# Performance work log

Measured on AMD Instinct MI355X. Metric: run time of the kernel, lower is better.

The kernel has to match this reference:

```python
import jax, jax.numpy as jnp
import numpy as np

H, C = 8, 16           # heads, per-head channels
NEG_SLOPE = 0.2        # PyG GATConv leaky_relu slope
N_NODES, N_EDGES, F_IN, N_GRAPHS = 50000, 600000, 64, 500


def setup_inputs() -> dict:
    key = jax.random.key(0)
    ks = jax.random.split(key, 24)
    s = 0.1  # weight init scale
    inp = {
        "x": jax.random.normal(ks[0], (N_NODES, F_IN), jnp.float32),
        "edge_index": jax.random.randint(ks[1], (2, N_EDGES), 0, N_NODES, dtype=jnp.int64),
        "batch": jnp.sort(jax.random.randint(ks[2], (N_NODES,), 0, N_GRAPHS, dtype=jnp.int64)),
        "W1": jax.random.normal(ks[3], (F_IN, H * C), jnp.float32) * s,
        "as1": jax.random.normal(ks[4], (H, C), jnp.float32) * s,
        "ad1": jax.random.normal(ks[5], (H, C), jnp.float32) * s,
        "b1": jnp.zeros((H * C,), jnp.float32),
        "W2": jax.random.normal(ks[6], (H * C, H * C), jnp.float32) * s,
        "as2": jax.random.normal(ks[7], (H, C), jnp.float32) * s,
        "ad2": jax.random.normal(ks[8], (H, C), jnp.float32) * s,
        "b2": jnp.zeros((H * C,), jnp.float32),
        "W3": jax.random.normal(ks[9], (H * C, H * C), jnp.float32) * s,
        "as3": jax.random.normal(ks[10], (H, C), jnp.float32) * s,
        "ad3": jax.random.normal(ks[11], (H, C), jnp.float32) * s,
        "b3": jnp.zeros((H * C,), jnp.float32),
        "fc1_w": jax.random.normal(ks[12], (H * C, 10), jnp.float32) * s,
        "fc1_b": jnp.zeros((10,), jnp.float32),
        "fc2_w": jax.random.normal(ks[13], (10, 1), jnp.float32) * s,
        "fc2_b": jnp.zeros((1,), jnp.float32),
    }
    return inp


def gat_layer(x, src, dst, W, att_src, att_dst, bias, n):
    # x: [N, F_in] -> h: [N, H, C]
    h = (x @ W).reshape(n, H, C)
    a_src = jnp.sum(h * att_src, axis=-1)  # [N, H]
    a_dst = jnp.sum(h * att_dst, axis=-1)  # [N, H]
    e = jax.nn.leaky_relu(a_src[src] + a_dst[dst], NEG_SLOPE)  # [E, H]
    # per-destination segment softmax (numerically stable)
    m = jax.ops.segment_max(e, dst, num_segments=n)            # [N, H]
    e = jnp.exp(e - m[dst])
    z = jax.ops.segment_sum(e, dst, num_segments=n)            # [N, H]
    alpha = e / (z[dst] + 1e-16)                               # [E, H]
    out = jax.ops.segment_sum(h[src] * alpha[:, :, None], dst, num_segments=n)  # [N, H, C]
    return out.reshape(n, H * C) + bias


def reference(x, edge_index, batch, W1, as1, ad1, b1, W2, as2, ad2, b2,
              W3, as3, ad3, b3, fc1_w, fc1_b, fc2_w, fc2_b):
    n = x.shape[0]
    # PyG GATConv default add_self_loops=True
    loop = jnp.arange(n, dtype=edge_index.dtype)
    src = jnp.concatenate([edge_index[0], loop])
    dst = jnp.concatenate([edge_index[1], loop])

    x = jax.nn.relu(gat_layer(x, src, dst, W1, as1, ad1, b1, n))
    x = jax.nn.relu(gat_layer(x, src, dst, W2, as2, ad2, b2, n))
    x = jax.nn.relu(gat_layer(x, src, dst, W3, as3, ad3, b3, n))

    # global_mean_pool over graphs
    sums = jax.ops.segment_sum(x, batch, num_segments=N_GRAPHS)          # [G, 128]
    cnts = jax.ops.segment_sum(jnp.ones((n,), x.dtype), batch, num_segments=N_GRAPHS)
    pooled = sums / jnp.maximum(cnts, 1.0)[:, None]

    hdn = jax.nn.relu(pooled @ fc1_w + fc1_b)
    return hdn @ fc2_w + fc2_b  # [G, 1]
```

## Files before the change

### kernel.cpp

```cpp
#include <hip/hip_runtime.h>
#include <hip/hip_bf16.h>

#define H 8
#define C 16
#define HC 128
#define NEG_SLOPE 0.2f

__global__ void init_kernel(int* __restrict__ deg8, int n) {
    int i = blockIdx.x * 256 + threadIdx.x;
    if (i < n) deg8[i] = 0;
}

__global__ void hist8_gptr_kernel(const int* __restrict__ ei, const int* __restrict__ batch,
                                  int* __restrict__ deg8, int* __restrict__ gptr,
                                  int E, int N, int G) {
    int t = blockIdx.x * 256 + threadIdx.x;
    int* dg = deg8 + (size_t)(blockIdx.x & 7) * N;
    int e0 = t * 4;
    if (e0 + 3 < E) {
        int4 d4 = *(const int4*)(ei + E + e0);
        atomicAdd(&dg[d4.x], 1);
        atomicAdd(&dg[d4.y], 1);
        atomicAdd(&dg[d4.z], 1);
        atomicAdd(&dg[d4.w], 1);
    } else if (e0 < E) {
        for (int j = e0; j < E; ++j) atomicAdd(&dg[ei[E + j]], 1);
    }
    int n0 = t * 4;
    if (n0 < N) {
        int v0 = batch[n0];
        int v1 = (n0 + 1 < N) ? batch[n0 + 1] : v0;
        int v2 = (n0 + 2 < N) ? batch[n0 + 2] : v1;
        int v3 = (n0 + 3 < N) ? batch[n0 + 3] : v2;
        int vals[4] = {v0, v1, v2, v3};
        int prev = (n0 == 0) ? -1 : batch[n0 - 1];
        for (int j = 0; j < 4; ++j) {
            int i = n0 + j;
            if (i >= N) break;
            int cur = vals[j];
            if (cur != prev)
                for (int g = prev + 1; g <= cur; ++g) gptr[g] = i;
            if (i == N - 1)
                for (int g = cur + 1; g <= G; ++g) gptr[g] = N;
            prev = cur;
        }
    }
}

__global__ void deg_reduce_kernel(const int* __restrict__ deg8, int* __restrict__ deg, int N) {
    int d = blockIdx.x * 256 + threadIdx.x;
    if (d >= N) return;
    int s = 1;
#pragma unroll
    for (int c = 0; c < 8; ++c) s += deg8[(size_t)c * N + d];
    deg[d] = s;
}

__global__ void scan_blk_kernel(const int* __restrict__ a, int* __restrict__ o,
                                int* __restrict__ p, int n) {
    __shared__ int sh[256];
    int tid = threadIdx.x;
    int base = blockIdx.x * 1024 + tid * 4;
    int4 v = make_int4(0, 0, 0, 0);
    if (base + 3 < n) v = *(const int4*)(a + base);
    else {
        if (base < n)     v.x = a[base];
        if (base + 1 < n) v.y = a[base + 1];
        if (base + 2 < n) v.z = a[base + 2];
        if (base + 3 < n) v.w = a[base + 3];
    }
    v.x = (v.x + 7) & ~7; v.y = (v.y + 7) & ~7; v.z = (v.z + 7) & ~7; v.w = (v.w + 7) & ~7;
    if (base >= n)     v.x = 0;
    if (base + 1 >= n) v.y = 0;
    if (base + 2 >= n) v.z = 0;
    if (base + 3 >= n) v.w = 0;
    int s = v.x + v.y + v.z + v.w;
    sh[tid] = s;
    __syncthreads();
    for (int off = 1; off < 256; off <<= 1) {
        int t = (tid >= off) ? sh[tid - off] : 0;
        __syncthreads();
        sh[tid] += t;
        __syncthreads();
    }
    int excl = sh[tid] - s;
    int4 ov;
    ov.x = excl; ov.y = ov.x + v.x; ov.z = ov.y + v.y; ov.w = ov.z + v.z;
    if (base + 3 < n) *(int4*)(o + base) = ov;
    else {
        if (base < n)     o[base] = ov.x;
        if (base + 1 < n) o[base + 1] = ov.y;
        if (base + 2 < n) o[base + 2] = ov.z;
        if (base + 3 < n) o[base + 3] = ov.w;
    }
    if (tid == 255) p[blockIdx.x] = sh[255];
}

__global__ void scan_part_kernel(int* __restrict__ p, int* __restrict__ tot, int nb) {
    __shared__ int sh[256];
    int tid = threadIdx.x;
    int v = (tid < nb) ? p[tid] : 0;
    sh[tid] = v;
    __syncthreads();
    for (int off = 1; off < 256; off <<= 1) {
        int t = (tid >= off) ? sh[tid - off] : 0;
        __syncthreads();
        sh[tid] += t;
        __syncthreads();
    }
    if (tid < nb) p[tid] = sh[tid] - v;
    if (tid == 255) *tot = sh[255];
}

__global__ void scan_add_kernel(int* __restrict__ o, const int* __restrict__ p, int n) {
    int off = p[blockIdx.x];
    int base = blockIdx.x * 1024 + threadIdx.x * 4;
    if (base + 3 < n) {
        int4 v = *(const int4*)(o + base);
        v.x += off; v.y += off; v.z += off; v.w += off;
        *(int4*)(o + base) = v;
    } else {
        if (base < n)     o[base] += off;
        if (base + 1 < n) o[base + 1] += off;
        if (base + 2 < n) o[base + 2] += off;
        if (base + 3 < n) o[base + 3] += off;
    }
}

__global__ void base_fill_kernel(int* __restrict__ deg8 ,
                                 const int* __restrict__ rowptr, int* __restrict__ csr, int N) {
    int d = blockIdx.x * 256 + threadIdx.x;
    if (d >= N) return;
    int base = rowptr[d];
    csr[base] = d;
    int run = base + 1;
    int cnt[8];
#pragma unroll
    for (int c = 0; c < 8; ++c) cnt[c] = deg8[(size_t)c * N + d];
#pragma unroll
    for (int c = 0; c < 8; ++c) { deg8[(size_t)c * N + d] = run; run += cnt[c]; }
    int rend = rowptr[d + 1];
    for (int p = run; p < rend; ++p) csr[p] = N;
    if (d == 0) {
        int tot = rowptr[N];
        for (int k = 0; k < 64; ++k) csr[tot + k] = N;
    }
}

__global__ void scatter8_kernel(const int* __restrict__ ei, int* __restrict__ base8,
                                int* __restrict__ csr, int E, int N) {
    int t = blockIdx.x * 256 + threadIdx.x;
    int* cur = base8 + (size_t)(blockIdx.x & 7) * N;
    int e0 = t * 4;
    if (e0 + 3 < E) {
        int4 s4 = *(const int4*)(ei + e0);
        int4 d4 = *(const int4*)(ei + E + e0);
        int p;
        p = atomicAdd(&cur[d4.x], 1); csr[p] = s4.x;
        p = atomicAdd(&cur[d4.y], 1); csr[p] = s4.y;
        p = atomicAdd(&cur[d4.z], 1); csr[p] = s4.z;
        p = atomicAdd(&cur[d4.w], 1); csr[p] = s4.w;
    } else if (e0 < E) {
        for (int j = e0; j < E; ++j) {
            int p = atomicAdd(&cur[ei[E + j]], 1);
            csr[p] = ei[j];
        }
    }
}

template <int K>
__global__ void gemm_att_kernel(const float* __restrict__ x, const float* __restrict__ W,
                                const float* __restrict__ as_, const float* __restrict__ ad_,
                                float* __restrict__ h, float* __restrict__ asrc,
                                float* __restrict__ adst, int n) {
    const int ROWS = 64;
    __shared__ float xs[ROWS][HC];
    int tx = threadIdx.x & 31;
    int ty = threadIdx.x >> 5;
    int row0 = blockIdx.x * ROWS;

    if (blockIdx.x == 0) {
        if (threadIdx.x < HC) h[(size_t)n * HC + threadIdx.x] = 0.f;
        if (threadIdx.x < H)  asrc[(size_t)n * H + threadIdx.x] = -INFINITY;
    }

    const int NV = ROWS * K / 4;
    for (int idx = threadIdx.x; idx < NV; idx += 256) {
        int rr = idx / (K / 4), kk = idx % (K / 4);
        int gr = row0 + rr;
        float4 v = (gr < n) ? ((const float4*)(x + (size_t)gr * K))[kk]
                            : make_float4(0.f, 0.f, 0.f, 0.f);
        *(float4*)(&xs[rr][kk * 4]) = v;
    }
    __syncthreads();

    const float* Wc = W + tx * 4;
    float acc[8][4];
#pragma unroll
    for (int r = 0; r < 8; ++r)
#pragma unroll
        for (int c = 0; c < 4; ++c) acc[r][c] = 0.f;

    for (int k = 0; k < K; k += 4) {
        float4 wv[4];
#pragma unroll
        for (int kk = 0; kk < 4; ++kk)
            wv[kk] = *(const float4*)(Wc + (size_t)(k + kk) * HC);
#pragma unroll
        for (int r = 0; r < 8; ++r) {
            float4 xr = *(const float4*)(&xs[ty * 8 + r][k]);
            acc[r][0] = fmaf(xr.x, wv[0].x, acc[r][0]);
            acc[r][1] = fmaf(xr.x, wv[0].y, acc[r][1]);
            acc[r][2] = fmaf(xr.x, wv[0].z, acc[r][2]);
            acc[r][3] = fmaf(xr.x, wv[0].w, acc[r][3]);
            acc[r][0] = fmaf(xr.y, wv[1].x, acc[r][0]);
            acc[r][1] = fmaf(xr.y, wv[1].y, acc[r][1]);
            acc[r][2] = fmaf(xr.y, wv[1].z, acc[r][2]);
            acc[r][3] = fmaf(xr.y, wv[1].w, acc[r][3]);
            acc[r][0] = fmaf(xr.z, wv[2].x, acc[r][0]);
            acc[r][1] = fmaf(xr.z, wv[2].y, acc[r][1]);
            acc[r][2] = fmaf(xr.z, wv[2].z, acc[r][2]);
            acc[r][3] = fmaf(xr.z, wv[2].w, acc[r][3]);
            acc[r][0] = fmaf(xr.w, wv[3].x, acc[r][0]);
            acc[r][1] = fmaf(xr.w, wv[3].y, acc[r][1]);
            acc[r][2] = fmaf(xr.w, wv[3].z, acc[r][2]);
            acc[r][3] = fmaf(xr.w, wv[3].w, acc[r][3]);
        }
    }
    __syncthreads();
#pragma unroll
    for (int r = 0; r < 8; ++r) {
        float4 o = make_float4(acc[r][0], acc[r][1], acc[r][2], acc[r][3]);
        *(float4*)(&xs[ty * 8 + r][tx * 4]) = o;
        int row = row0 + ty * 8 + r;
        if (row < n) *(float4*)(h + (size_t)row * HC + tx * 4) = o;
    }
    __syncthreads();

#pragma unroll
    for (int rep = 0; rep < 2; ++rep) {
        int pidx = threadIdx.x + rep * 256;
        int row = pidx >> 3;
        int hd = pidx & 7;
        if (row0 + row < n) {
            const float4* hv = (const float4*)&xs[row][hd * 16];
            const float4* sv = (const float4*)(as_ + hd * 16);
            const float4* dv = (const float4*)(ad_ + hd * 16);
            float s = 0.f, d = 0.f;
#pragma unroll
            for (int j = 0; j < 4; ++j) {
                float4 a = hv[j], u = sv[j], v = dv[j];
                s += a.x * u.x + a.y * u.y + a.z * u.z + a.w * u.w;
                d += a.x * v.x + a.y * v.y + a.z * v.z + a.w * v.w;
            }
            asrc[(size_t)(row0 + row) * H + hd] = s;
            adst[(size_t)(row0 + row) * H + hd] = d;
        }
    }
}

__global__ void gat_agg_kernel(const int* __restrict__ rowptr, const int* __restrict__ csr_src,
                               const float* __restrict__ h, const float* __restrict__ asrc,
                               const float* __restrict__ adst, const float* __restrict__ bias,
                               float* __restrict__ out, int N) {
    int dst = (blockIdx.x * 256 + threadIdx.x) >> 6;
    if (dst >= N) return;
    int lane = threadIdx.x & 63;
    int hd = lane >> 3;
    int beg = rowptr[dst], end = rowptr[dst + 1];
    float ad = adst[(size_t)dst * H + hd];
    const float2* h2 = (const float2*)h;

    float z = 0.f, a0 = 0.f, a1 = 0.f;
    int i0, i1, i2, i3, i4, i5, i6, i7;
    float e0, e1, e2, e3, e4, e5, e6, e7;
    float2 v0, v1, v2, v3, v4, v5, v6, v7;

#define LOADI(S, J) i##S = csr_src[(J)];
#define LOADV(S)                                                           \
    { e##S = asrc[(size_t)i##S * H + hd]; v##S = h2[(size_t)i##S * 64 + lane]; }
#define PROCE(S)                                                           \
    {   float e = e##S + ad;                                               \
        e = e > 0.f ? e : NEG_SLOPE * e;                                   \
        float w = __expf(e);                                               \
        z += w;                                                            \
        a0 = fmaf(w, v##S.x, a0);                                          \
        a1 = fmaf(w, v##S.y, a1);                                          \
    }
    LOADI(0, beg)     LOADI(1, beg + 1) LOADI(2, beg + 2) LOADI(3, beg + 3)
    LOADI(4, beg + 4) LOADI(5, beg + 5) LOADI(6, beg + 6) LOADI(7, beg + 7)
    LOADV(0) LOADV(1) LOADV(2) LOADV(3) LOADV(4) LOADV(5) LOADV(6) LOADV(7)
    LOADI(0, beg + 8)  LOADI(1, beg + 9)  LOADI(2, beg + 10) LOADI(3, beg + 11)
    LOADI(4, beg + 12) LOADI(5, beg + 13) LOADI(6, beg + 14) LOADI(7, beg + 15)

    for (int j = beg; j < end; j += 8) {
        PROCE(0) LOADV(0)
        PROCE(1) LOADV(1)
        PROCE(2) LOADV(2)
        PROCE(3) LOADV(3)
        PROCE(4) LOADV(4)
        PROCE(5) LOADV(5)
        PROCE(6) LOADV(6)
        PROCE(7) LOADV(7)
        LOADI(0, j + 16) LOADI(1, j + 17) LOADI(2, j + 18) LOADI(3, j + 19)
        LOADI(4, j + 20) LOADI(5, j + 21) LOADI(6, j + 22) LOADI(7, j + 23)
    }
#undef LOADI
#undef LOADV
#undef PROCE
    float inv = 1.f / (z + 1e-16f);
    int c2 = lane * 2;
    float r0 = fmaxf(a0 * inv + bias[c2], 0.f);
    float r1 = fmaxf(a1 * inv + bias[c2 + 1], 0.f);
    *(float2*)(out + (size_t)dst * HC + c2) = make_float2(r0, r1);
}

__global__ void pool_mlp_kernel(const float* __restrict__ x, const int* __restrict__ gptr,
                                const float* __restrict__ fc1w, const float* __restrict__ fc1b,
                                const float* __restrict__ fc2w, const float* __restrict__ fc2b,
                                float* __restrict__ out, int G) {
    __shared__ float sp[HC];
    __shared__ float sh[10];
    int g = blockIdx.x;
    int c = threadIdx.x;
    int beg = gptr[g], end = gptr[g + 1];
    float acc = 0.f;
    for (int n = beg; n < end; ++n) acc += x[(size_t)n * HC + c];
    sp[c] = acc / fmaxf((float)(end - beg), 1.f);
    __syncthreads();
    if (c < 10) {
        float s = fc1b[c];
        for (int k = 0; k < HC; ++k) s = fmaf(sp[k], fc1w[k * 10 + c], s);
        sh[c] = fmaxf(s, 0.f);
    }
    __syncthreads();
    if (c == 0) {
        float o = fc2b[0];
#pragma unroll
        for (int j = 0; j < 10; ++j) o = fmaf(sh[j], fc2w[j], o);
        out[g] = o;
    }
}

extern "C" void kernel_launch(void* const* d_in, const int* in_sizes, int n_in,
                              void* d_out, int out_size, void* d_ws, size_t ws_size,
                              hipStream_t stream) {
    const int N = in_sizes[0] / 64;
    const int E = in_sizes[1] / 2;
    const int G = out_size;
    const int CSR_CAP = E + 8 * N + 64;

    const float* x     = (const float*)d_in[0];
    const int*   ei    = (const int*)d_in[1];
    const int*   batch = (const int*)d_in[2];
    const float* W1 = (const float*)d_in[3];
    const float* as1 = (const float*)d_in[4];
    const float* ad1 = (const float*)d_in[5];
    const float* b1 = (const float*)d_in[6];
    const float* W2 = (const float*)d_in[7];
    const float* as2 = (const float*)d_in[8];
    const float* ad2 = (const float*)d_in[9];
    const float* b2 = (const float*)d_in[10];
    const float* W3 = (const float*)d_in[11];
    const float* as3 = (const float*)d_in[12];
    const float* ad3 = (const float*)d_in[13];
    const float* b3 = (const float*)d_in[14];
    const float* fc1w = (const float*)d_in[15];
    const float* fc1b = (const float*)d_in[16];
    const float* fc2w = (const float*)d_in[17];
    const float* fc2b = (const float*)d_in[18];

    float* ws = (float*)d_ws;
    float* h    = ws;
    float* xb0  = h + (size_t)(N + 1) * HC;
    float* xb1  = xb0 + (size_t)N * HC;
    float* asrc = xb1 + (size_t)N * HC;
    float* adst = asrc + (size_t)(N + 1) * H;
    int* ints   = (int*)(adst + (size_t)N * H);
    int* deg8   = ints;
    int* deg    = deg8 + (size_t)8 * N;
    int* rowptr = deg + N;
    int* gptr   = rowptr + N + 16;
    int* partN  = gptr + G + 16;
    int* csr    = partN + 256;

    dim3 blk(256);
    int grid4   = ((E + 3) / 4 + 255) / 256;
    int grid_n  = (N + 255) / 256;
    int grid_agg = (N * 64 + 255) / 256;
    int nbN = (N + 1023) / 1024;

    init_kernel<<<(8 * N + 255) / 256, blk, 0, stream>>>(deg8, 8 * N);
    hist8_gptr_kernel<<<grid4, blk, 0, stream>>>(ei, batch, deg8, gptr, E, N, G);
    deg_reduce_kernel<<<grid_n, blk, 0, stream>>>(deg8, deg, N);
    scan_blk_kernel<<<nbN, blk, 0, stream>>>(deg, rowptr, partN, N);
    scan_part_kernel<<<1, blk, 0, stream>>>(partN, rowptr + N, nbN);
    scan_add_kernel<<<nbN, blk, 0, stream>>>(rowptr, partN, N);
    base_fill_kernel<<<grid_n, blk, 0, stream>>>(deg8, rowptr, csr, N);
    scatter8_kernel<<<grid4, blk, 0, stream>>>(ei, deg8, csr, E, N);

    auto run_layer = [&](const float* xin, int K, const float* W, const float* as_,
                         const float* ad_, const float* b, float* out) {
        if (K == 64)
            gemm_att_kernel<64><<<(N + 63) / 64, blk, 0, stream>>>(xin, W, as_, ad_,
                                                                   h, asrc, adst, N);
        else
            gemm_att_kernel<128><<<(N + 63) / 64, blk, 0, stream>>>(xin, W, as_, ad_,
                                                                    h, asrc, adst, N);
        gat_agg_kernel<<<grid_agg, blk, 0, stream>>>(rowptr, csr, h, asrc, adst, b, out, N);
    };

    run_layer(x,   64,  W1, as1, ad1, b1, xb0);
    run_layer(xb0, 128, W2, as2, ad2, b2, xb1);
    run_layer(xb1, 128, W3, as3, ad3, b3, xb0);

    pool_mlp_kernel<<<G, dim3(128), 0, stream>>>(xb0, gptr, fc1w, fc1b, fc2w, fc2b,
                                                 (float*)d_out, G);
}
```

Before: 366.0 us.

## Widen aggregation software pipeline to 16 edges and double-buffer GEMM weight loads

```diff
diff --git a/kernel.cpp b/kernel.cpp
--- a/kernel.cpp
+++ b/kernel.cpp
@@ -69,7 +69,8 @@
         if (base + 2 < n) v.z = a[base + 2];
         if (base + 3 < n) v.w = a[base + 3];
     }
-    v.x = (v.x + 7) & ~7; v.y = (v.y + 7) & ~7; v.z = (v.z + 7) & ~7; v.w = (v.w + 7) & ~7;
+    v.x = (v.x + 15) & ~15; v.y = (v.y + 15) & ~15;
+    v.z = (v.z + 15) & ~15; v.w = (v.w + 15) & ~15;
     if (base >= n)     v.x = 0;
     if (base + 1 >= n) v.y = 0;
     if (base + 2 >= n) v.z = 0;
@@ -201,11 +202,17 @@
 #pragma unroll
         for (int c = 0; c < 4; ++c) acc[r][c] = 0.f;
 
+    float4 wv[4], wn[4];
+#pragma unroll
+    for (int kk = 0; kk < 4; ++kk)
+        wv[kk] = *(const float4*)(Wc + (size_t)kk * HC);
+
     for (int k = 0; k < K; k += 4) {
-        float4 wv[4];
-#pragma unroll
-        for (int kk = 0; kk < 4; ++kk)
-            wv[kk] = *(const float4*)(Wc + (size_t)(k + kk) * HC);
+        if (k + 4 < K) {
+#pragma unroll
+            for (int kk = 0; kk < 4; ++kk)
+                wn[kk] = *(const float4*)(Wc + (size_t)(k + 4 + kk) * HC);
+        }
 #pragma unroll
         for (int r = 0; r < 8; ++r) {
             float4 xr = *(const float4*)(&xs[ty * 8 + r][k]);
@@ -226,6 +233,8 @@
             acc[r][2] = fmaf(xr.w, wv[3].z, acc[r][2]);
             acc[r][3] = fmaf(xr.w, wv[3].w, acc[r][3]);
         }
+#pragma unroll
+        for (int kk = 0; kk < 4; ++kk) wv[kk] = wn[kk];
     }
     __syncthreads();
 #pragma unroll
@@ -272,9 +281,9 @@
     const float2* h2 = (const float2*)h;
 
     float z = 0.f, a0 = 0.f, a1 = 0.f;
-    int i0, i1, i2, i3, i4, i5, i6, i7;
-    float e0, e1, e2, e3, e4, e5, e6, e7;
-    float2 v0, v1, v2, v3, v4, v5, v6, v7;
+    int i0, i1, i2, i3, i4, i5, i6, i7, i8, i9, i10, i11, i12, i13, i14, i15;
+    float e0, e1, e2, e3, e4, e5, e6, e7, e8, e9, e10, e11, e12, e13, e14, e15;
+    float2 v0, v1, v2, v3, v4, v5, v6, v7, v8, v9, v10, v11, v12, v13, v14, v15;
 
 #define LOADI(S, J) i##S = csr_src[(J)];
 #define LOADV(S)                                                           \
@@ -287,27 +296,43 @@
         a0 = fmaf(w, v##S.x, a0);                                          \
         a1 = fmaf(w, v##S.y, a1);                                          \
     }
-    LOADI(0, beg)     LOADI(1, beg + 1) LOADI(2, beg + 2) LOADI(3, beg + 3)
-    LOADI(4, beg + 4) LOADI(5, beg + 5) LOADI(6, beg + 6) LOADI(7, beg + 7)
-    LOADV(0) LOADV(1) LOADV(2) LOADV(3) LOADV(4) LOADV(5) LOADV(6) LOADV(7)
-    LOADI(0, beg + 8)  LOADI(1, beg + 9)  LOADI(2, beg + 10) LOADI(3, beg + 11)
-    LOADI(4, beg + 12) LOADI(5, beg + 13) LOADI(6, beg + 14) LOADI(7, beg + 15)
-
-    for (int j = beg; j < end; j += 8) {
-        PROCE(0) LOADV(0)
-        PROCE(1) LOADV(1)
-        PROCE(2) LOADV(2)
-        PROCE(3) LOADV(3)
-        PROCE(4) LOADV(4)
-        PROCE(5) LOADV(5)
-        PROCE(6) LOADV(6)
-        PROCE(7) LOADV(7)
-        LOADI(0, j + 16) LOADI(1, j + 17) LOADI(2, j + 18) LOADI(3, j + 19)
-        LOADI(4, j + 20) LOADI(5, j + 21) LOADI(6, j + 22) LOADI(7, j + 23)
+#define LOADI_G(B)                                                          \
+    LOADI(0,(B))      LOADI(1,(B)+1)   LOADI(2,(B)+2)   LOADI(3,(B)+3)     \
+    LOADI(4,(B)+4)    LOADI(5,(B)+5)   LOADI(6,(B)+6)   LOADI(7,(B)+7)     \
+    LOADI(8,(B)+8)    LOADI(9,(B)+9)   LOADI(10,(B)+10) LOADI(11,(B)+11)   \
+    LOADI(12,(B)+12)  LOADI(13,(B)+13) LOADI(14,(B)+14) LOADI(15,(B)+15)
+#define LOADV_G                                                             \
+    LOADV(0)  LOADV(1)  LOADV(2)  LOADV(3)  LOADV(4)  LOADV(5)  LOADV(6)  LOADV(7) \
+    LOADV(8)  LOADV(9)  LOADV(10) LOADV(11) LOADV(12) LOADV(13) LOADV(14) LOADV(15)
+
+    LOADI_G(beg)
+    LOADV_G
+    LOADI_G(beg + 16)
+
+    for (int j = beg; j < end; j += 16) {
+        PROCE(0)  LOADV(0)
+        PROCE(1)  LOADV(1)
+        PROCE(2)  LOADV(2)
+        PROCE(3)  LOADV(3)
+        PROCE(4)  LOADV(4)
+        PROCE(5)  LOADV(5)
+        PROCE(6)  LOADV(6)
+        PROCE(7)  LOADV(7)
+        PROCE(8)  LOADV(8)
+        PROCE(9)  LOADV(9)
+        PROCE(10) LOADV(10)
+        PROCE(11) LOADV(11)
+        PROCE(12) LOADV(12)
+        PROCE(13) LOADV(13)
+        PROCE(14) LOADV(14)
+        PROCE(15) LOADV(15)
+        LOADI_G(j + 32)
     }
 #undef LOADI
 #undef LOADV
 #undef PROCE
+#undef LOADI_G
+#undef LOADV_G
     float inv = 1.f / (z + 1e-16f);
     int c2 = lane * 2;
     float r0 = fmaxf(a0 * inv + bias[c2], 0.f);
@@ -348,7 +373,7 @@
     const int N = in_sizes[0] / 64;
     const int E = in_sizes[1] / 2;
     const int G = out_size;
-    const int CSR_CAP = E + 8 * N + 64;
+    const int CSR_CAP = E + 16 * N + 64;
 
     const float* x     = (const float*)d_in[0];
     const int*   ei    = (const int*)d_in[1];
```

New measurement: 372.0 us. About the same (+1.6%).
